# Performance work log

Hardware: AMD Instinct MI355X
Metric: run time of the kernel (lower is better)

Reference implementation:

```python
import jax, jax.numpy as jnp
import numpy as np

M = 12      # max_context_size
H = 768     # hidden_size
NH = 8      # global encoder heads
HD = H // NH
FF = 2048   # global encoder ff_dim
B = 8192


def _gather_hist(buf, mask, idx, ctx):
    """Age-sorted gather of valid circular-buffer slots (oldest first), padded to ctx."""
    Bb, Mx, Hh = buf.shape
    pos = jnp.arange(Mx)
    age = (idx[:, None] - pos[None, :]) % Mx              # [B,M] age of each slot
    key = jnp.where(mask, -age, Mx + 1)                   # valid slots first, oldest (max age) first
    order = jnp.argsort(key, axis=1)                      # stable sort, matches python sorted()
    sorted_buf = jnp.take_along_axis(buf, order[:, :, None], axis=1)
    nvalid = mask.sum(axis=1)                             # [B]
    hist = sorted_buf[:, :ctx]                            # [B,ctx,H]
    valid = jnp.arange(ctx)[None, :] < nvalid[:, None]
    hist = hist * valid[:, :, None]                       # zero out padding rows
    return hist, jnp.minimum(nvalid, ctx)


def _seq_with_current(buf, mask, idx, z_k, ctx):
    """History (ctx-1 slots) + current utterance at the last position (faithful to original,
    including the original's padding-mask behavior arange >= hist_len+1)."""
    Bb = z_k.shape[0]
    hist, hlen = _gather_hist(buf, mask, idx, ctx - 1)
    seq = jnp.concatenate([hist, jnp.zeros((Bb, 1, buf.shape[-1]), buf.dtype)], axis=1)
    seq = seq.at[:, ctx - 1].set(z_k)
    lengths = jnp.minimum(hlen + 1, ctx)
    pad = jnp.arange(ctx)[None, :] >= lengths[:, None]    # True = padded
    return seq, lengths, pad


def _layernorm(x, g, b):
    mu = x.mean(-1, keepdims=True)
    var = x.var(-1, keepdims=True)
    return (x - mu) * jax.lax.rsqrt(var + 1e-5) * g + b


def _forward(z_k, context_buffer, buffer_mask, buffer_indices,
             Wq, bq, Wk, bk, Wv, bv, Wo, bo, ln1_g, ln1_b,
             W1, b1, W2, b2, ln2_g, ln2_b, Wd, bd, Wl, bl, Wg, bg):
    mask = buffer_mask.astype(bool)
    idx = buffer_indices.astype(jnp.int32)
    Bb = z_k.shape[0]

    # ---- global path: 12-slot context -> post-LN transformer layer -> masked mean pool
    gseq, glen, gpad = _seq_with_current(context_buffer, mask, idx, z_k, 12)
    S = 12
    q = (gseq @ Wq + bq).reshape(Bb, S, NH, HD)
    k = (gseq @ Wk + bk).reshape(Bb, S, NH, HD)
    v = (gseq @ Wv + bv).reshape(Bb, S, NH, HD)
    scores = jnp.einsum('bqhd,bkhd->bhqk', q, k) / np.sqrt(HD).astype(np.float32)
    scores = jnp.where(gpad[:, None, None, :], jnp.float32(-1e9), scores)
    attn = jax.nn.softmax(scores, axis=-1)
    ao = jnp.einsum('bhqk,bkhd->bqhd', attn, v).reshape(Bb, S, H) @ Wo + bo
    x = _layernorm(gseq + ao, ln1_g, ln1_b)
    ff = jax.nn.relu(x @ W1 + b1) @ W2 + b2
    x = _layernorm(x + ff, ln2_g, ln2_b)
    gvalid = (~gpad).astype(x.dtype)                       # [B,12]
    denom = jnp.maximum(gvalid.sum(1, keepdims=True), 1.0)
    x_g = (x * gvalid[:, :, None]).sum(1) / denom          # [B,H]

    # ---- direct path
    x_d = jnp.tanh(z_k @ Wd + bd)

    # ---- local path: 5-slot context -> masked mean pool -> projection
    lseq, llen, lpad = _seq_with_current(context_buffer, mask, idx, z_k, 5)
    lvalid = (~lpad).astype(lseq.dtype)
    ldenom = jnp.maximum(lvalid.sum(1, keepdims=True), 1.0)
    lpool = (lseq * lvalid[:, :, None]).sum(1) / ldenom
    x_l = jnp.tanh(lpool @ Wl + bl)

    # ---- gate over [direct, local, global]
    paths = jnp.stack([x_d, x_l, x_g], axis=1)             # [B,3,H]
    logits = paths.reshape(Bb, 3 * H) @ Wg + bg            # [B,3]
    gate = jax.nn.softmax(logits, axis=-1)
    h_k = jnp.einsum('br,brh->bh', gate, paths)
    return h_k


def setup_inputs() -> dict:
    key = jax.random.key(0)
    ks = jax.random.split(key, 24)
    s = 0.02
    inp = {
        'z_k': jax.random.normal(ks[0], (B, H), jnp.float32),
        'context_buffer': jax.random.normal(ks[1], (B, M, H), jnp.float32),
        'buffer_mask': jax.random.randint(ks[2], (B, M), 0, 2, jnp.int32),
        'buffer_indices': jax.random.randint(ks[3], (B,), 0, M, jnp.int32),
        'Wq': jax.random.normal(ks[4], (H, H), jnp.float32) * s,
        'bq': jnp.zeros((H,), jnp.float32),
        'Wk': jax.random.normal(ks[5], (H, H), jnp.float32) * s,
        'bk': jnp.zeros((H,), jnp.float32),
        'Wv': jax.random.normal(ks[6], (H, H), jnp.float32) * s,
        'bv': jnp.zeros((H,), jnp.float32),
        'Wo': jax.random.normal(ks[7], (H, H), jnp.float32) * s,
        'bo': jnp.zeros((H,), jnp.float32),
        'ln1_g': jnp.ones((H,), jnp.float32),
        'ln1_b': jnp.zeros((H,), jnp.float32),
        'W1': jax.random.normal(ks[8], (H, FF), jnp.float32) * s,
        'b1': jnp.zeros((FF,), jnp.float32),
        'W2': jax.random.normal(ks[9], (FF, H), jnp.float32) * s,
        'b2': jnp.zeros((H,), jnp.float32),
        'ln2_g': jnp.ones((H,), jnp.float32),
        'ln2_b': jnp.zeros((H,), jnp.float32),
        'Wd': jax.random.normal(ks[10], (H, H), jnp.float32) * s,
        'bd': jnp.zeros((H,), jnp.float32),
        'Wl': jax.random.normal(ks[11], (H, H), jnp.float32) * s,
        'bl': jnp.zeros((H,), jnp.float32),
        'Wg': jax.random.normal(ks[12], (3 * H, 3), jnp.float32) * s,
        'bg': jnp.zeros((3,), jnp.float32),
    }
    return inp


def reference(z_k, context_buffer, buffer_mask, buffer_indices,
              Wq, bq, Wk, bk, Wv, bv, Wo, bo, ln1_g, ln1_b,
              W1, b1, W2, b2, ln2_g, ln2_b, Wd, bd, Wl, bl, Wg, bg):
    return _forward(z_k, context_buffer, buffer_mask, buffer_indices,
                    Wq, bq, Wk, bk, Wv, bv, Wo, bo, ln1_g, ln1_b,
                    W1, b1, W2, b2, ln2_g, ln2_b, Wd, bd, Wl, bl, Wg, bg)
```

## Files before the change

### kernel.cpp

```cpp
#include <hip/hip_runtime.h>
#include <cstdint>
#include <cstddef>

typedef __bf16 bf16;
typedef __attribute__((ext_vector_type(8))) __bf16 bf16x8;
typedef __attribute__((ext_vector_type(4))) float f32x4;

#define B_TOT 8192

__device__ __forceinline__ void gload16(const void* g, void* l) {
  __builtin_amdgcn_global_load_lds(
      (__attribute__((address_space(1))) void*)g,
      (__attribute__((address_space(3))) void*)l, 16, 0, 0);
}

__device__ __forceinline__ void block_sum2(float& a, float& b, float* lds8) {
#pragma unroll
  for (int o = 32; o; o >>= 1) {
    a += __shfl_xor(a, o, 64);
    b += __shfl_xor(b, o, 64);
  }
  int w = threadIdx.x >> 6;
  if ((threadIdx.x & 63) == 0) { lds8[w] = a; lds8[4 + w] = b; }
  __syncthreads();
  a = lds8[0] + lds8[1] + lds8[2] + lds8[3];
  b = lds8[4] + lds8[5] + lds8[6] + lds8[7];
  __syncthreads();
}

__global__ __launch_bounds__(1024) void scan_kernel(
    const int* __restrict__ mask, int* __restrict__ Lg, int* __restrict__ base,
    int* __restrict__ meta, int b0, int Bc)
{
  __shared__ int tsum[1024];
  const int t = threadIdx.x;
  const int per = Bc >> 10;
  int l[8];
  int s = 0;
  for (int u = 0; u < per; ++u) {
    int b = t * per + u;
    const int* mp = mask + (long)(b0 + b) * 12;
    int nv = 0;
#pragma unroll
    for (int p = 0; p < 12; ++p) nv += (mp[p] != 0);
    int L = (nv < 11 ? nv : 11) + 1;
    l[u] = L; s += L;
  }
  tsum[t] = s;
  __syncthreads();
  for (int o = 1; o < 1024; o <<= 1) {
    int v = (t >= o) ? tsum[t - o] : 0;
    __syncthreads();
    tsum[t] += v;
    __syncthreads();
  }
  int excl = tsum[t] - s;
  for (int u = 0; u < per; ++u) {
    int b = t * per + u;
    Lg[b] = l[u];
    base[b] = excl;
    excl += l[u];
  }
  if (t == 1023) meta[0] = tsum[1023];
}

__global__ __launch_bounds__(256) void prep_kernel(
    const float* __restrict__ z, const float* __restrict__ buf,
    const int* __restrict__ mask, const int* __restrict__ idxs,
    const int* __restrict__ base, bf16* __restrict__ gseq,
    bf16* __restrict__ zl, int b0, int Bc)
{
  const int bl = blockIdx.x;
  const int b  = b0 + bl;
  __shared__ int ord[12];
  __shared__ int s_nv;
  if (threadIdx.x == 0) {
    int id = idxs[b];
    int nv = 0;
    for (int a = 11; a >= 0; --a) {
      int pos = id - a; if (pos < 0) pos += 12;
      if (mask[b * 12 + pos]) ord[nv++] = pos;
    }
    s_nv = nv;
  }
  __syncthreads();
  const int nv = s_nv;
  const int hg = (nv < 11 ? nv : 11);
  const int hl = (nv < 4 ? nv : 4);
  const long bs = base[bl];
  const float ld = 1.0f / (float)(hl + 1);
  for (int c = threadIdx.x; c < 768; c += 256) {
    float zv = z[(long)b * 768 + c];
    zl[(long)bl * 768 + c] = (bf16)zv;
    float ls = 0.0f;
    for (int s = 0; s < hg; ++s) {
      float v = buf[((long)b * 12 + ord[s]) * 768 + c];
      gseq[(bs + s) * 768 + c] = (bf16)v;
      if (s < hl) ls += v;
    }
    gseq[(bs + hg) * 768 + c] = (hg == 11) ? (bf16)zv : (bf16)0.0f;
    if (nv >= 4) ls += zv;
    zl[((long)Bc + bl) * 768 + c] = (bf16)(ls * ld);
  }
}

__global__ __launch_bounds__(256) void transpose_bf16(
    const float* __restrict__ W, bf16* __restrict__ Wt, int K, int N)
{
  __shared__ float tile[32][33];
  int bn = blockIdx.x * 32;
  int bk = blockIdx.y * 32;
  int tx = threadIdx.x & 31;
  int ty0 = threadIdx.x >> 5;
  for (int ty = ty0; ty < 32; ty += 8)
    tile[ty][tx] = W[(long)(bk + ty) * N + bn + tx];
  __syncthreads();
  for (int ty = ty0; ty < 32; ty += 8)
    Wt[(long)(bn + ty) * K + bk + tx] = (bf16)tile[tx][ty];
}

__global__ __launch_bounds__(256) void pack3_kernel(
    const float* __restrict__ a, const float* __restrict__ b,
    const float* __restrict__ c, float* __restrict__ out)
{
  int t = blockIdx.x * blockDim.x + threadIdx.x;
  if (t < 768) out[t] = a[t];
  else if (t < 1536) out[t] = b[t - 768];
  else if (t < 2304) out[t] = c[t - 1536];
}

__global__ __launch_bounds__(256, 2) void gemm_bt(
    const bf16* __restrict__ A, const bf16* __restrict__ Bt,
    const float* __restrict__ bias, void* __restrict__ C,
    int K, int N, int act, int outf32,
    const int* __restrict__ mlim, int msplit,
    const bf16* __restrict__ Bt2, const float* __restrict__ bias2)
{
  __shared__ __align__(16) bf16 As[128 * 32];
  __shared__ __align__(16) bf16 Bs[128 * 32];
  int gx = gridDim.x, gy = gridDim.y;
  int bx = blockIdx.x, by = blockIdx.y;
  if ((((gx * gy) & 7) == 0) && ((gy & 7) == 0)) {
    int l = bx + gx * by;
    int xcd = l & 7, slot = l >> 3;
    bx = slot % gx;
    by = (slot / gx) * 8 + xcd;
  }
  const long m0 = (long)by * 128;
  const long n0 = (long)bx * 128;
  if (mlim && m0 >= mlim[0]) return;
  const bf16* Bsel = (m0 >= msplit) ? Bt2 : Bt;
  const float* bsel = (m0 >= msplit) ? bias2 : bias;

  const int tid  = threadIdx.x;
  const int wave = tid >> 6;
  const int lane = tid & 63;
  const int wm = (wave >> 1) * 64;
  const int wn = (wave & 1) * 64;

  const int r0  = (wave * 2 + 0) * 16 + (lane >> 2);
  const int r1  = (wave * 2 + 1) * 16 + (lane >> 2);
  const int kc0 = (lane & 3) ^ ((r0 >> 1) & 3);
  const int kc1 = (lane & 3) ^ ((r1 >> 1) & 3);
  const bf16* Ag0 = A + (m0 + r0) * K + kc0 * 8;
  const bf16* Ag1 = A + (m0 + r1) * K + kc1 * 8;
  const bf16* Bg0 = Bsel + (n0 + r0) * K + kc0 * 8;
  const bf16* Bg1 = Bsel + (n0 + r1) * K + kc1 * 8;
  bf16* Al0 = As + (wave * 2 + 0) * 512 + lane * 8;
  bf16* Al1 = As + (wave * 2 + 1) * 512 + lane * 8;
  bf16* Bl0 = Bs + (wave * 2 + 0) * 512 + lane * 8;
  bf16* Bl1 = Bs + (wave * 2 + 1) * 512 + lane * 8;

  f32x4 acc[4][4] = {};
  const int i16  = lane & 15;
  const int quad = lane >> 4;

  for (int kt = 0; kt < K; kt += 32) {
    __syncthreads();
    gload16(Ag0 + kt, Al0);
    gload16(Ag1 + kt, Al1);
    gload16(Bg0 + kt, Bl0);
    gload16(Bg1 + kt, Bl1);
    __syncthreads();

    bf16x8 af[4], bfr[4];
#pragma unroll
    for (int i = 0; i < 4; ++i) {
      int r = wm + i * 16 + i16;
      af[i] = *(const bf16x8*)(As + r * 32 + ((quad ^ ((r >> 1) & 3)) * 8));
    }
#pragma unroll
    for (int j = 0; j < 4; ++j) {
      int r = wn + j * 16 + i16;
      bfr[j] = *(const bf16x8*)(Bs + r * 32 + ((quad ^ ((r >> 1) & 3)) * 8));
    }
#pragma unroll
    for (int i = 0; i < 4; ++i)
#pragma unroll
      for (int j = 0; j < 4; ++j)
        acc[i][j] = __builtin_amdgcn_mfma_f32_16x16x32_bf16(af[i], bfr[j], acc[i][j], 0, 0, 0);
  }

#pragma unroll
  for (int i = 0; i < 4; ++i) {
#pragma unroll
    for (int j = 0; j < 4; ++j) {
      long col = n0 + wn + j * 16 + i16;
      float bv = bsel[col];
#pragma unroll
      for (int r = 0; r < 4; ++r) {
        long row = m0 + wm + i * 16 + quad * 4 + r;
        float v = acc[i][j][r] + bv;
        if (act == 1) v = fmaxf(v, 0.0f);
        else if (act == 2) v = tanhf(v);
        if (outf32) ((float*)C)[row * N + col] = v;
        else        ((bf16*)C)[row * N + col] = (bf16)v;
      }
    }
  }
}

__global__ __launch_bounds__(256) void attn_kernel(
    const bf16* __restrict__ QKV, const int* __restrict__ base,
    const int* __restrict__ Lg, bf16* __restrict__ AO)
{
  const int bl  = blockIdx.x;
  const int tid = threadIdx.x;
  const int L   = Lg[bl];
  const long bs = base[bl];
  const bf16* qb = QKV + bs * 2304;
  __shared__ bf16 kx[12 * 776];
  __shared__ bf16 vx[12 * 776];
  __shared__ float att[8][12][12];
  const int LH = L * 768;
  for (int t = tid; t < LH; t += 256) {
    int s = t / 768, c = t - s * 768;
    kx[s * 776 + c] = qb[(long)s * 2304 + 768 + c];
    vx[s * 776 + c] = qb[(long)s * 2304 + 1536 + c];
  }
  __syncthreads();
  const int LL = L * L;
  for (int t = tid; t < 8 * LL; t += 256) {
    int h = t / LL, r = t - h * LL, i = r / L, j = r - (r / L) * L;
    const bf16x8* q = (const bf16x8*)(qb + (long)i * 2304 + h * 96);
    const bf16x8* k = (const bf16x8*)(kx + j * 776 + h * 96);
    float a = 0.0f;
#pragma unroll
    for (int d = 0; d < 12; ++d) {
      bf16x8 qa = q[d], ka = k[d];
#pragma unroll
      for (int e = 0; e < 8; ++e) a += (float)qa[e] * (float)ka[e];
    }
    att[h][i][j] = a * 0.10206207261596575f;
  }
  __syncthreads();
  for (int t = tid; t < 8 * L; t += 256) {
    int h = t / L, i = t - (t / L) * L;
    float mx = -3e38f;
    for (int j = 0; j < L; ++j) mx = fmaxf(mx, att[h][i][j]);
    float sum = 0.0f;
    for (int j = 0; j < L; ++j) { float e = __expf(att[h][i][j] - mx); att[h][i][j] = e; sum += e; }
    float inv = 1.0f / sum;
    for (int j = 0; j < L; ++j) att[h][i][j] *= inv;
  }
  __syncthreads();
  for (int t = tid; t < LH; t += 256) {
    int i = t / 768, c = t - i * 768, h = c / 96;
    float a = 0.0f;
    for (int j = 0; j < L; ++j) a += att[h][i][j] * (float)vx[j * 776 + c];
    AO[(bs + i) * 768 + c] = (bf16)a;
  }
}

__global__ __launch_bounds__(256) void ln1_kernel(
    const bf16* __restrict__ WoO, const bf16* __restrict__ gseq,
    const float* __restrict__ gam, const float* __restrict__ bet,
    bf16* __restrict__ X, const int* __restrict__ meta)
{
  const long row = blockIdx.x;
  if (row >= meta[0]) return;
  const int tid = threadIdx.x;
  __shared__ float red[8];
  float v[3]; float s = 0.0f, ss = 0.0f;
#pragma unroll
  for (int u = 0; u < 3; ++u) {
    int c = tid + u * 256;
    float x = (float)WoO[row * 768 + c] + (float)gseq[row * 768 + c];
    v[u] = x; s += x; ss += x * x;
  }
  block_sum2(s, ss, red);
  float mu  = s * (1.0f / 768.0f);
  float var = ss * (1.0f / 768.0f) - mu * mu;
  float inv = 1.0f / sqrtf(var + 1e-5f);
#pragma unroll
  for (int u = 0; u < 3; ++u) {
    int c = tid + u * 256;
    X[row * 768 + c] = (bf16)((v[u] - mu) * inv * gam[c] + bet[c]);
  }
}

__global__ __launch_bounds__(256) void ln2pool_kernel(
    const bf16* __restrict__ X, const bf16* __restrict__ FFo,
    const float* __restrict__ gam, const float* __restrict__ bet,
    const int* __restrict__ base, const int* __restrict__ Lg,
    float* __restrict__ xg)
{
  const int bl = blockIdx.x;
  const int tid = threadIdx.x;
  const int L = Lg[bl];
  const long bs = base[bl];
  __shared__ float red[8];
  float p0 = 0.0f, p1 = 0.0f, p2 = 0.0f;
  for (int s = 0; s < L; ++s) {
    long row = bs + s;
    float v[3]; float sm = 0.0f, sq = 0.0f;
#pragma unroll
    for (int u = 0; u < 3; ++u) {
      int c = tid + u * 256;
      float x = (float)X[row * 768 + c] + (float)FFo[row * 768 + c];
      v[u] = x; sm += x; sq += x * x;
    }
    block_sum2(sm, sq, red);
    float mu  = sm * (1.0f / 768.0f);
    float var = sq * (1.0f / 768.0f) - mu * mu;
    float inv = 1.0f / sqrtf(var + 1e-5f);
    p0 += (v[0] - mu) * inv * gam[tid]       + bet[tid];
    p1 += (v[1] - mu) * inv * gam[tid + 256] + bet[tid + 256];
    p2 += (v[2] - mu) * inv * gam[tid + 512] + bet[tid + 512];
  }
  float dn = 1.0f / (float)L;
  xg[(long)bl * 768 + tid]       = p0 * dn;
  xg[(long)bl * 768 + tid + 256] = p1 * dn;
  xg[(long)bl * 768 + tid + 512] = p2 * dn;
}

__global__ __launch_bounds__(256) void final_kernel(
    const float* __restrict__ xdl, const float* __restrict__ xg,
    const float* __restrict__ Wg, const float* __restrict__ bg,
    float* __restrict__ out, int b0, int Bc)
{
  const int bl = blockIdx.x;
  const int tid = threadIdx.x;
  __shared__ float red[12];
  const float* xd = xdl + (long)bl * 768;
  const float* xl = xdl + ((long)Bc + bl) * 768;
  const float* xgp = xg + (long)bl * 768;
  float l0 = 0.0f, l1 = 0.0f, l2 = 0.0f;
  for (int u = tid; u < 768; u += 256) {
    float pd = xd[u], pl = xl[u], pg = xgp[u];
    l0 += pd * Wg[u * 3 + 0] + pl * Wg[(u + 768) * 3 + 0] + pg * Wg[(u + 1536) * 3 + 0];
    l1 += pd * Wg[u * 3 + 1] + pl * Wg[(u + 768) * 3 + 1] + pg * Wg[(u + 1536) * 3 + 1];
    l2 += pd * Wg[u * 3 + 2] + pl * Wg[(u + 768) * 3 + 2] + pg * Wg[(u + 1536) * 3 + 2];
  }
#pragma unroll
  for (int o = 32; o; o >>= 1) {
    l0 += __shfl_xor(l0, o, 64);
    l1 += __shfl_xor(l1, o, 64);
    l2 += __shfl_xor(l2, o, 64);
  }
  if ((tid & 63) == 0) { int w = tid >> 6; red[w * 3] = l0; red[w * 3 + 1] = l1; red[w * 3 + 2] = l2; }
  __syncthreads();
  l0 = red[0] + red[3] + red[6] + red[9]  + bg[0];
  l1 = red[1] + red[4] + red[7] + red[10] + bg[1];
  l2 = red[2] + red[5] + red[8] + red[11] + bg[2];
  float mx = fmaxf(l0, fmaxf(l1, l2));
  float e0 = __expf(l0 - mx), e1 = __expf(l1 - mx), e2 = __expf(l2 - mx);
  float inv = 1.0f / (e0 + e1 + e2);
  e0 *= inv; e1 *= inv; e2 *= inv;
  for (int u = tid; u < 768; u += 256) {
    out[((long)(b0 + bl)) * 768 + u] = e0 * xd[u] + e1 * xl[u] + e2 * xgp[u];
  }
}

extern "C" void kernel_launch(void* const* d_in, const int* in_sizes, int n_in,
                              void* d_out, int out_size, void* d_ws, size_t ws_size,
                              hipStream_t stream) {
  const float* z    = (const float*)d_in[0];
  const float* buf  = (const float*)d_in[1];
  const int*   mask = (const int*)d_in[2];
  const int*   idxs = (const int*)d_in[3];
  const float* Wq = (const float*)d_in[4];  const float* bq = (const float*)d_in[5];
  const float* Wk = (const float*)d_in[6];  const float* bk = (const float*)d_in[7];
  const float* Wv = (const float*)d_in[8];  const float* bv = (const float*)d_in[9];
  const float* Wo = (const float*)d_in[10]; const float* bo = (const float*)d_in[11];
  const float* ln1g = (const float*)d_in[12]; const float* ln1b = (const float*)d_in[13];
  const float* W1 = (const float*)d_in[14]; const float* b1 = (const float*)d_in[15];
  const float* W2 = (const float*)d_in[16]; const float* b2 = (const float*)d_in[17];
  const float* ln2g = (const float*)d_in[18]; const float* ln2b = (const float*)d_in[19];
  const float* Wd = (const float*)d_in[20]; const float* bd = (const float*)d_in[21];
  const float* Wl = (const float*)d_in[22]; const float* blw = (const float*)d_in[23];
  const float* Wg = (const float*)d_in[24]; const float* bg = (const float*)d_in[25];
  float* out = (float*)d_out;
  (void)in_sizes; (void)n_in; (void)out_size;

  auto rnd = [](size_t x) { return (x + 255) & ~(size_t)255; };

  size_t fixed = 0;
  fixed += rnd((size_t)2304 * 768 * 2);
  fixed += rnd((size_t)768 * 768 * 2);
  fixed += rnd((size_t)2048 * 768 * 2);
  fixed += rnd((size_t)768 * 2048 * 2);
  fixed += rnd((size_t)768 * 768 * 2) * 2;
  fixed += rnd((size_t)2304 * 4) + 256;

  auto chunkBytes = [&](size_t bc) {
    return rnd((size_t)55296 * bc) + 3 * rnd((size_t)18432 * bc)
         + rnd((size_t)3072 * bc) + rnd((size_t)6144 * bc) + rnd((size_t)3072 * bc)
         + 2 * rnd((size_t)4 * bc);
  };
  int Bc = 8192;
  while (Bc > 1024 && fixed + chunkBytes(Bc) > ws_size) Bc >>= 1;

  size_t off = 0;
  auto alloc = [&](size_t n) { void* p = (char*)d_ws + off; off += rnd(n); return p; };
  bf16* Wqkv_t = (bf16*)alloc((size_t)2304 * 768 * 2);
  bf16* Wo_t   = (bf16*)alloc((size_t)768 * 768 * 2);
  bf16* W1_t   = (bf16*)alloc((size_t)2048 * 768 * 2);
  bf16* W2_t   = (bf16*)alloc((size_t)768 * 2048 * 2);
  bf16* Wd_t   = (bf16*)alloc((size_t)768 * 768 * 2);
  bf16* Wl_t   = (bf16*)alloc((size_t)768 * 768 * 2);
  float* bqkv  = (float*)alloc((size_t)2304 * 4);
  int*  meta   = (int*)alloc(256);
  bf16* P1 = (bf16*)alloc((size_t)55296 * Bc);
  bf16* P2 = (bf16*)alloc((size_t)18432 * Bc);
  bf16* P3 = (bf16*)alloc((size_t)18432 * Bc);
  bf16* P4 = (bf16*)alloc((size_t)18432 * Bc);
  bf16* zl   = (bf16*)alloc((size_t)3072 * Bc);
  float* xdl = (float*)alloc((size_t)6144 * Bc);
  float* xg  = (float*)alloc((size_t)3072 * Bc);
  int*  Lg   = (int*)alloc((size_t)4 * Bc);
  int*  base = (int*)alloc((size_t)4 * Bc);

  transpose_bf16<<<dim3(24, 24), 256, 0, stream>>>(Wq, Wqkv_t,                 768, 768);
  transpose_bf16<<<dim3(24, 24), 256, 0, stream>>>(Wk, Wqkv_t + 768 * 768,     768, 768);
  transpose_bf16<<<dim3(24, 24), 256, 0, stream>>>(Wv, Wqkv_t + 2 * 768 * 768, 768, 768);
  transpose_bf16<<<dim3(24, 24), 256, 0, stream>>>(Wo, Wo_t, 768, 768);
  transpose_bf16<<<dim3(64, 24), 256, 0, stream>>>(W1, W1_t, 768, 2048);
  transpose_bf16<<<dim3(24, 64), 256, 0, stream>>>(W2, W2_t, 2048, 768);
  transpose_bf16<<<dim3(24, 24), 256, 0, stream>>>(Wd, Wd_t, 768, 768);
  transpose_bf16<<<dim3(24, 24), 256, 0, stream>>>(Wl, Wl_t, 768, 768);
  pack3_kernel<<<9, 256, 0, stream>>>(bq, bk, bv, bqkv);

  const int BIG = 0x7fffffff;
  for (int b0 = 0; b0 < B_TOT; b0 += Bc) {
    const int Ycap = (12 * Bc) / 128;
    scan_kernel<<<1, 1024, 0, stream>>>(mask, Lg, base, meta, b0, Bc);
    prep_kernel<<<Bc, 256, 0, stream>>>(z, buf, mask, idxs, base, P2, zl, b0, Bc);
    gemm_bt<<<dim3(18, Ycap), 256, 0, stream>>>(P2, Wqkv_t, bqkv, P1, 768, 2304, 0, 0, meta, BIG, nullptr, nullptr);
    attn_kernel<<<Bc, 256, 0, stream>>>(P1, base, Lg, P3);
    gemm_bt<<<dim3(6, Ycap), 256, 0, stream>>>(P3, Wo_t, bo, P4, 768, 768, 0, 0, meta, BIG, nullptr, nullptr);
    ln1_kernel<<<12 * Bc, 256, 0, stream>>>(P4, P2, ln1g, ln1b, P3, meta);
    gemm_bt<<<dim3(16, Ycap), 256, 0, stream>>>(P3, W1_t, b1, P1, 768, 2048, 1, 0, meta, BIG, nullptr, nullptr);
    gemm_bt<<<dim3(6, Ycap), 256, 0, stream>>>(P1, W2_t, b2, P2, 2048, 768, 0, 0, meta, BIG, nullptr, nullptr);
    ln2pool_kernel<<<Bc, 256, 0, stream>>>(P3, P2, ln2g, ln2b, base, Lg, xg);
    gemm_bt<<<dim3(6, (2 * Bc) / 128), 256, 0, stream>>>(zl, Wd_t, bd, xdl, 768, 768, 2, 1, nullptr, Bc, Wl_t, blw);
    final_kernel<<<Bc, 256, 0, stream>>>(xdl, xg, Wg, bg, out, b0, Bc);
  }
}
```

Before: 1.798 ms.

## Widen GEMM K-tile, stage bf16 epilogue via LDS, parallelize scan, fuse pooling with gate

The GEMM now loads 64-wide K tiles per barrier pair with an XOR swizzle, which halves the number of sync rounds. Its bf16 epilogue stages the output tile in LDS so global stores are coalesced 16-byte writes. The single-block 1024-thread scan becomes a two-level scan, with prep_kernel folding in the block offsets. The LN2/pool kernel is fused with the softmax gating kernel, removing the xg buffer round trip and one launch, and the local/dense GEMM is moved earlier in the stream. LDS use per GEMM block doubles, which may affect occupancy.

```diff
diff --git a/kernel.cpp b/kernel.cpp
--- a/kernel.cpp
+++ b/kernel.cpp
@@ -28,46 +28,46 @@
   __syncthreads();
 }
 
-__global__ __launch_bounds__(1024) void scan_kernel(
-    const int* __restrict__ mask, int* __restrict__ Lg, int* __restrict__ base,
-    int* __restrict__ meta, int b0, int Bc)
-{
-  __shared__ int tsum[1024];
+__global__ __launch_bounds__(256) void scan1_kernel(
+    const int* __restrict__ mask, int* __restrict__ Lg, int* __restrict__ lbase,
+    int* __restrict__ btot, int b0)
+{
+  __shared__ int ts[256];
   const int t = threadIdx.x;
-  const int per = Bc >> 10;
-  int l[8];
-  int s = 0;
-  for (int u = 0; u < per; ++u) {
-    int b = t * per + u;
-    const int* mp = mask + (long)(b0 + b) * 12;
-    int nv = 0;
-#pragma unroll
-    for (int p = 0; p < 12; ++p) nv += (mp[p] != 0);
-    int L = (nv < 11 ? nv : 11) + 1;
-    l[u] = L; s += L;
-  }
-  tsum[t] = s;
-  __syncthreads();
-  for (int o = 1; o < 1024; o <<= 1) {
-    int v = (t >= o) ? tsum[t - o] : 0;
-    __syncthreads();
-    tsum[t] += v;
-    __syncthreads();
-  }
-  int excl = tsum[t] - s;
-  for (int u = 0; u < per; ++u) {
-    int b = t * per + u;
-    Lg[b] = l[u];
-    base[b] = excl;
-    excl += l[u];
-  }
-  if (t == 1023) meta[0] = tsum[1023];
+  const int b = blockIdx.x * 256 + t;
+  const int* mp = mask + (long)(b0 + b) * 12;
+  int nv = 0;
+#pragma unroll
+  for (int p = 0; p < 12; ++p) nv += (mp[p] != 0);
+  int L = (nv < 11 ? nv : 11) + 1;
+  ts[t] = L;
+  __syncthreads();
+  for (int o = 1; o < 256; o <<= 1) {
+    int v = (t >= o) ? ts[t - o] : 0;
+    __syncthreads();
+    ts[t] += v;
+    __syncthreads();
+  }
+  Lg[b] = L;
+  lbase[b] = ts[t] - L;
+  if (t == 255) btot[blockIdx.x] = ts[255];
+}
+
+__global__ __launch_bounds__(64) void scan2_kernel(
+    const int* __restrict__ btot, int* __restrict__ boff, int* __restrict__ meta, int nb)
+{
+  if (threadIdx.x == 0) {
+    int acc = 0;
+    for (int i = 0; i < nb; ++i) { int v = btot[i]; boff[i] = acc; acc += v; }
+    meta[0] = acc;
+  }
 }
 
 __global__ __launch_bounds__(256) void prep_kernel(
     const float* __restrict__ z, const float* __restrict__ buf,
     const int* __restrict__ mask, const int* __restrict__ idxs,
-    const int* __restrict__ base, bf16* __restrict__ gseq,
+    const int* __restrict__ lbase, const int* __restrict__ boff,
+    int* __restrict__ fbase, bf16* __restrict__ gseq,
     bf16* __restrict__ zl, int b0, int Bc)
 {
   const int bl = blockIdx.x;
@@ -83,11 +83,12 @@
     }
     s_nv = nv;
   }
+  const long bs = (long)lbase[bl] + boff[bl >> 8];
+  if (threadIdx.x == 0) fbase[bl] = (int)bs;
   __syncthreads();
   const int nv = s_nv;
   const int hg = (nv < 11 ? nv : 11);
   const int hl = (nv < 4 ? nv : 4);
-  const long bs = base[bl];
   const float ld = 1.0f / (float)(hl + 1);
   for (int c = threadIdx.x; c < 768; c += 256) {
     float zv = z[(long)b * 768 + c];
@@ -136,11 +137,12 @@
     const int* __restrict__ mlim, int msplit,
     const bf16* __restrict__ Bt2, const float* __restrict__ bias2)
 {
-  __shared__ __align__(16) bf16 As[128 * 32];
-  __shared__ __align__(16) bf16 Bs[128 * 32];
+  __shared__ __align__(16) bf16 smem[2 * 128 * 64];
+  bf16* As = smem;
+  bf16* Bs = smem + 128 * 64;
   int gx = gridDim.x, gy = gridDim.y;
   int bx = blockIdx.x, by = blockIdx.y;
-  if ((((gx * gy) & 7) == 0) && ((gy & 7) == 0)) {
+  if ((gy & 7) == 0) {
     int l = bx + gx * by;
     int xcd = l & 7, slot = l >> 3;
     bx = slot % gx;
@@ -157,77 +159,109 @@
   const int lane = tid & 63;
   const int wm = (wave >> 1) * 64;
   const int wn = (wave & 1) * 64;
-
-  const int r0  = (wave * 2 + 0) * 16 + (lane >> 2);
-  const int r1  = (wave * 2 + 1) * 16 + (lane >> 2);
-  const int kc0 = (lane & 3) ^ ((r0 >> 1) & 3);
-  const int kc1 = (lane & 3) ^ ((r1 >> 1) & 3);
-  const bf16* Ag0 = A + (m0 + r0) * K + kc0 * 8;
-  const bf16* Ag1 = A + (m0 + r1) * K + kc1 * 8;
-  const bf16* Bg0 = Bsel + (n0 + r0) * K + kc0 * 8;
-  const bf16* Bg1 = Bsel + (n0 + r1) * K + kc1 * 8;
-  bf16* Al0 = As + (wave * 2 + 0) * 512 + lane * 8;
-  bf16* Al1 = As + (wave * 2 + 1) * 512 + lane * 8;
-  bf16* Bl0 = Bs + (wave * 2 + 0) * 512 + lane * 8;
-  bf16* Bl1 = Bs + (wave * 2 + 1) * 512 + lane * 8;
-
-  f32x4 acc[4][4] = {};
   const int i16  = lane & 15;
   const int quad = lane >> 4;
-
-  for (int kt = 0; kt < K; kt += 32) {
-    __syncthreads();
-    gload16(Ag0 + kt, Al0);
-    gload16(Ag1 + kt, Al1);
-    gload16(Bg0 + kt, Bl0);
-    gload16(Bg1 + kt, Bl1);
-    __syncthreads();
-
-    bf16x8 af[4], bfr[4];
+  const int l8 = lane >> 3;
+  const int c7 = lane & 7;
+
+  const int csrc = c7 ^ l8;
+  const bf16* Ag[4]; const bf16* Bg[4];
+  bf16* Al[4]; bf16* Bl[4];
+#pragma unroll
+  for (int u = 0; u < 4; ++u) {
+    int r = wave * 32 + u * 8 + l8;
+    Ag[u] = A    + (m0 + r) * K + csrc * 8;
+    Bg[u] = Bsel + (n0 + r) * K + csrc * 8;
+    Al[u] = As + (wave * 32 + u * 8) * 64 + lane * 8;
+    Bl[u] = Bs + (wave * 32 + u * 8) * 64 + lane * 8;
+  }
+
+  f32x4 acc[4][4] = {};
+
+  for (int kt = 0; kt < K; kt += 64) {
+    __syncthreads();
+#pragma unroll
+    for (int u = 0; u < 4; ++u) {
+      gload16(Ag[u] + kt, Al[u]);
+      gload16(Bg[u] + kt, Bl[u]);
+    }
+    __syncthreads();
+#pragma unroll
+    for (int s = 0; s < 2; ++s) {
+      const int cofs = ((s << 2) | quad) ^ c7;
+      bf16x8 af[4], bfr[4];
+#pragma unroll
+      for (int i = 0; i < 4; ++i)
+        af[i] = *(const bf16x8*)(As + (wm + i * 16 + i16) * 64 + cofs * 8);
+#pragma unroll
+      for (int j = 0; j < 4; ++j)
+        bfr[j] = *(const bf16x8*)(Bs + (wn + j * 16 + i16) * 64 + cofs * 8);
+#pragma unroll
+      for (int i = 0; i < 4; ++i)
+#pragma unroll
+        for (int j = 0; j < 4; ++j)
+          acc[i][j] = __builtin_amdgcn_mfma_f32_16x16x32_bf16(af[i], bfr[j], acc[i][j], 0, 0, 0);
+    }
+  }
+
+  if (!outf32) {
+    __syncthreads();
+    bf16* Cs = smem;
+#pragma unroll
+    for (int j = 0; j < 4; ++j) {
+      int col = wn + j * 16 + i16;
+      int c8s = (col >> 3) ^ (quad << 1);
+      int clo = col & 7;
+      float bv = bsel[n0 + col];
+#pragma unroll
+      for (int i = 0; i < 4; ++i) {
+#pragma unroll
+        for (int r = 0; r < 4; ++r) {
+          int row = wm + i * 16 + quad * 4 + r;
+          float v = acc[i][j][r] + bv;
+          if (act == 1) v = fmaxf(v, 0.0f);
+          Cs[row * 128 + c8s * 8 + clo] = (bf16)v;
+        }
+      }
+    }
+    __syncthreads();
+    bf16* Cg = (bf16*)C;
+#pragma unroll
+    for (int u = 0; u < 8; ++u) {
+      int g = u * 256 + tid;
+      int row = g >> 4, c8 = g & 15;
+      int c8s = c8 ^ (((row >> 2) & 3) << 1);
+      *(bf16x8*)(Cg + (m0 + row) * N + n0 + c8 * 8) =
+          *(const bf16x8*)(Cs + row * 128 + c8s * 8);
+    }
+  } else {
 #pragma unroll
     for (int i = 0; i < 4; ++i) {
-      int r = wm + i * 16 + i16;
-      af[i] = *(const bf16x8*)(As + r * 32 + ((quad ^ ((r >> 1) & 3)) * 8));
-    }
-#pragma unroll
-    for (int j = 0; j < 4; ++j) {
-      int r = wn + j * 16 + i16;
-      bfr[j] = *(const bf16x8*)(Bs + r * 32 + ((quad ^ ((r >> 1) & 3)) * 8));
-    }
-#pragma unroll
-    for (int i = 0; i < 4; ++i)
-#pragma unroll
-      for (int j = 0; j < 4; ++j)
-        acc[i][j] = __builtin_amdgcn_mfma_f32_16x16x32_bf16(af[i], bfr[j], acc[i][j], 0, 0, 0);
-  }
-
-#pragma unroll
-  for (int i = 0; i < 4; ++i) {
-#pragma unroll
-    for (int j = 0; j < 4; ++j) {
-      long col = n0 + wn + j * 16 + i16;
-      float bv = bsel[col];
-#pragma unroll
-      for (int r = 0; r < 4; ++r) {
-        long row = m0 + wm + i * 16 + quad * 4 + r;
-        float v = acc[i][j][r] + bv;
-        if (act == 1) v = fmaxf(v, 0.0f);
-        else if (act == 2) v = tanhf(v);
-        if (outf32) ((float*)C)[row * N + col] = v;
-        else        ((bf16*)C)[row * N + col] = (bf16)v;
+#pragma unroll
+      for (int j = 0; j < 4; ++j) {
+        long col = n0 + wn + j * 16 + i16;
+        float bv = bsel[col];
+#pragma unroll
+        for (int r = 0; r < 4; ++r) {
+          long row = m0 + wm + i * 16 + quad * 4 + r;
+          float v = acc[i][j][r] + bv;
+          if (act == 1) v = fmaxf(v, 0.0f);
+          else if (act == 2) v = tanhf(v);
+          ((float*)C)[row * N + col] = v;
+        }
       }
     }
   }
 }
 
 __global__ __launch_bounds__(256) void attn_kernel(
-    const bf16* __restrict__ QKV, const int* __restrict__ base,
+    const bf16* __restrict__ QKV, const int* __restrict__ fbase,
     const int* __restrict__ Lg, bf16* __restrict__ AO)
 {
   const int bl  = blockIdx.x;
   const int tid = threadIdx.x;
   const int L   = Lg[bl];
-  const long bs = base[bl];
+  const long bs = fbase[bl];
   const bf16* qb = QKV + bs * 2304;
   __shared__ bf16 kx[12 * 776];
   __shared__ bf16 vx[12 * 776];
@@ -299,17 +333,19 @@
   }
 }
 
-__global__ __launch_bounds__(256) void ln2pool_kernel(
+__global__ __launch_bounds__(256) void ln2gate_kernel(
     const bf16* __restrict__ X, const bf16* __restrict__ FFo,
     const float* __restrict__ gam, const float* __restrict__ bet,
-    const int* __restrict__ base, const int* __restrict__ Lg,
-    float* __restrict__ xg)
+    const int* __restrict__ fbase, const int* __restrict__ Lg,
+    const float* __restrict__ xdl, const float* __restrict__ Wg,
+    const float* __restrict__ bg, float* __restrict__ out, int b0, int Bc)
 {
   const int bl = blockIdx.x;
   const int tid = threadIdx.x;
   const int L = Lg[bl];
-  const long bs = base[bl];
+  const long bs = fbase[bl];
   __shared__ float red[8];
+  __shared__ float red3[12];
   float p0 = 0.0f, p1 = 0.0f, p2 = 0.0f;
   for (int s = 0; s < L; ++s) {
     long row = bs + s;
@@ -329,28 +365,18 @@
     p2 += (v[2] - mu) * inv * gam[tid + 512] + bet[tid + 512];
   }
   float dn = 1.0f / (float)L;
-  xg[(long)bl * 768 + tid]       = p0 * dn;
-  xg[(long)bl * 768 + tid + 256] = p1 * dn;
-  xg[(long)bl * 768 + tid + 512] = p2 * dn;
-}
-
-__global__ __launch_bounds__(256) void final_kernel(
-    const float* __restrict__ xdl, const float* __restrict__ xg,
-    const float* __restrict__ Wg, const float* __restrict__ bg,
-    float* __restrict__ out, int b0, int Bc)
-{
-  const int bl = blockIdx.x;
-  const int tid = threadIdx.x;
-  __shared__ float red[12];
+  p0 *= dn; p1 *= dn; p2 *= dn;
   const float* xd = xdl + (long)bl * 768;
   const float* xl = xdl + ((long)Bc + bl) * 768;
-  const float* xgp = xg + (long)bl * 768;
+  float xd0 = xd[tid], xd1 = xd[tid + 256], xd2 = xd[tid + 512];
+  float xl0 = xl[tid], xl1 = xl[tid + 256], xl2 = xl[tid + 512];
   float l0 = 0.0f, l1 = 0.0f, l2 = 0.0f;
-  for (int u = tid; u < 768; u += 256) {
-    float pd = xd[u], pl = xl[u], pg = xgp[u];
-    l0 += pd * Wg[u * 3 + 0] + pl * Wg[(u + 768) * 3 + 0] + pg * Wg[(u + 1536) * 3 + 0];
-    l1 += pd * Wg[u * 3 + 1] + pl * Wg[(u + 768) * 3 + 1] + pg * Wg[(u + 1536) * 3 + 1];
-    l2 += pd * Wg[u * 3 + 2] + pl * Wg[(u + 768) * 3 + 2] + pg * Wg[(u + 1536) * 3 + 2];
+#pragma unroll
+  for (int r = 0; r < 3; ++r) {
+    float lr = xd0 * Wg[tid * 3 + r] + xd1 * Wg[(tid + 256) * 3 + r] + xd2 * Wg[(tid + 512) * 3 + r]
+             + xl0 * Wg[(768 + tid) * 3 + r] + xl1 * Wg[(1024 + tid) * 3 + r] + xl2 * Wg[(1280 + tid) * 3 + r]
+             + p0 * Wg[(1536 + tid) * 3 + r] + p1 * Wg[(1792 + tid) * 3 + r] + p2 * Wg[(2048 + tid) * 3 + r];
+    if (r == 0) l0 = lr; else if (r == 1) l1 = lr; else l2 = lr;
   }
 #pragma unroll
   for (int o = 32; o; o >>= 1) {
@@ -358,18 +384,19 @@
     l1 += __shfl_xor(l1, o, 64);
     l2 += __shfl_xor(l2, o, 64);
   }
-  if ((tid & 63) == 0) { int w = tid >> 6; red[w * 3] = l0; red[w * 3 + 1] = l1; red[w * 3 + 2] = l2; }
-  __syncthreads();
-  l0 = red[0] + red[3] + red[6] + red[9]  + bg[0];
-  l1 = red[1] + red[4] + red[7] + red[10] + bg[1];
-  l2 = red[2] + red[5] + red[8] + red[11] + bg[2];
+  if ((tid & 63) == 0) { int w = tid >> 6; red3[w * 3] = l0; red3[w * 3 + 1] = l1; red3[w * 3 + 2] = l2; }
+  __syncthreads();
+  l0 = red3[0] + red3[3] + red3[6] + red3[9]  + bg[0];
+  l1 = red3[1] + red3[4] + red3[7] + red3[10] + bg[1];
+  l2 = red3[2] + red3[5] + red3[8] + red3[11] + bg[2];
   float mx = fmaxf(l0, fmaxf(l1, l2));
   float e0 = __expf(l0 - mx), e1 = __expf(l1 - mx), e2 = __expf(l2 - mx);
   float inv = 1.0f / (e0 + e1 + e2);
   e0 *= inv; e1 *= inv; e2 *= inv;
-  for (int u = tid; u < 768; u += 256) {
-    out[((long)(b0 + bl)) * 768 + u] = e0 * xd[u] + e1 * xl[u] + e2 * xgp[u];
-  }
+  float* op = out + (long)(b0 + bl) * 768;
+  op[tid]       = e0 * xd0 + e1 * xl0 + e2 * p0;
+  op[tid + 256] = e0 * xd1 + e1 * xl1 + e2 * p1;
+  op[tid + 512] = e0 * xd2 + e1 * xl2 + e2 * p2;
 }
 
 extern "C" void kernel_launch(void* const* d_in, const int* in_sizes, int n_in,
@@ -401,12 +428,12 @@
   fixed += rnd((size_t)2048 * 768 * 2);
   fixed += rnd((size_t)768 * 2048 * 2);
   fixed += rnd((size_t)768 * 768 * 2) * 2;
-  fixed += rnd((size_t)2304 * 4) + 256;
+  fixed += rnd((size_t)2304 * 4) + 256 + 512 + 512;
 
   auto chunkBytes = [&](size_t bc) {
     return rnd((size_t)55296 * bc) + 3 * rnd((size_t)18432 * bc)
-         + rnd((size_t)3072 * bc) + rnd((size_t)6144 * bc) + rnd((size_t)3072 * bc)
-         + 2 * rnd((size_t)4 * bc);
+         + rnd((size_t)3072 * bc) + rnd((size_t)6144 * bc)
+         + 3 * rnd((size_t)4 * bc);
   };
   int Bc = 8192;
   while (Bc > 1024 && fixed + chunkBytes(Bc) > ws_size) Bc >>= 1;
@@ -421,15 +448,17 @@
   bf16* Wl_t   = (bf16*)alloc((size_t)768 * 768 * 2);
   float* bqkv  = (float*)alloc((size_t)2304 * 4);
   int*  meta   = (int*)alloc(256);
+  int*  btot   = (int*)alloc(512);
+  int*  boff   = (int*)alloc(512);
   bf16* P1 = (bf16*)alloc((size_t)55296 * Bc);
   bf16* P2 = (bf16*)alloc((size_t)18432 * Bc);
   bf16* P3 = (bf16*)alloc((size_t)18432 * Bc);
   bf16* P4 = (bf16*)alloc((size_t)18432 * Bc);
   bf16* zl   = (bf16*)alloc((size_t)3072 * Bc);
   float* xdl = (float*)alloc((size_t)6144 * Bc);
-  float* xg  = (float*)alloc((size_t)3072 * Bc);
-  int*  Lg   = (int*)alloc((size_t)4 * Bc);
-  int*  base = (int*)alloc((size_t)4 * Bc);
+  int*  Lg    = (int*)alloc((size_t)4 * Bc);
+  int*  lbase = (int*)alloc((size_t)4 * Bc);
+  int*  fbase = (int*)alloc((size_t)4 * Bc);
 
   transpose_bf16<<<dim3(24, 24), 256, 0, stream>>>(Wq, Wqkv_t,                 768, 768);
   transpose_bf16<<<dim3(24, 24), 256, 0, stream>>>(Wk, Wqkv_t + 768 * 768,     768, 768);
@@ -444,16 +473,16 @@
   const int BIG = 0x7fffffff;
   for (int b0 = 0; b0 < B_TOT; b0 += Bc) {
     const int Ycap = (12 * Bc) / 128;
-    scan_kernel<<<1, 1024, 0, stream>>>(mask, Lg, base, meta, b0, Bc);
-    prep_kernel<<<Bc, 256, 0, stream>>>(z, buf, mask, idxs, base, P2, zl, b0, Bc);
+    scan1_kernel<<<Bc / 256, 256, 0, stream>>>(mask, Lg, lbase, btot, b0);
+    scan2_kernel<<<1, 64, 0, stream>>>(btot, boff, meta, Bc / 256);
+    prep_kernel<<<Bc, 256, 0, stream>>>(z, buf, mask, idxs, lbase, boff, fbase, P2, zl, b0, Bc);
+    gemm_bt<<<dim3(6, (2 * Bc) / 128), 256, 0, stream>>>(zl, Wd_t, bd, xdl, 768, 768, 2, 1, nullptr, Bc, Wl_t, blw);
     gemm_bt<<<dim3(18, Ycap), 256, 0, stream>>>(P2, Wqkv_t, bqkv, P1, 768, 2304, 0, 0, meta, BIG, nullptr, nullptr);
-    attn_kernel<<<Bc, 256, 0, stream>>>(P1, base, Lg, P3);
+    attn_kernel<<<Bc, 256, 0, stream>>>(P1, fbase, Lg, P3);
     gemm_bt<<<dim3(6, Ycap), 256, 0, stream>>>(P3, Wo_t, bo, P4, 768, 768, 0, 0, meta, BIG, nullptr, nullptr);
     ln1_kernel<<<12 * Bc, 256, 0, stream>>>(P4, P2, ln1g, ln1b, P3, meta);
     gemm_bt<<<dim3(16, Ycap), 256, 0, stream>>>(P3, W1_t, b1, P1, 768, 2048, 1, 0, meta, BIG, nullptr, nullptr);
     gemm_bt<<<dim3(6, Ycap), 256, 0, stream>>>(P1, W2_t, b2, P2, 2048, 768, 0, 0, meta, BIG, nullptr, nullptr);
-    ln2pool_kernel<<<Bc, 256, 0, stream>>>(P3, P2, ln2g, ln2b, base, Lg, xg);
-    gemm_bt<<<dim3(6, (2 * Bc) / 128), 256, 0, stream>>>(zl, Wd_t, bd, xdl, 768, 768, 2, 1, nullptr, Bc, Wl_t, blw);
-    final_kernel<<<Bc, 256, 0, stream>>>(xdl, xg, Wg, bg, out, b0, Bc);
-  }
-}
+    ln2gate_kernel<<<Bc, 256, 0, stream>>>(P3, P2, ln2g, ln2b, fbase, Lg, xdl, Wg, bg, out, b0, Bc);
+  }
+}
```

Result: faster. 1.592 ms (-11.5%).
